# Kernel tuning notes

Measured on AMD Instinct MI355X. Metric: run time of the kernel, lower is better.

Reference implementation:

```python
import jax, jax.numpy as jnp
import numpy as np

EMBD = 512
HEADS = 8
HEAD = EMBD // HEADS


def setup_inputs() -> dict:
    key = jax.random.key(0)
    ks = jax.random.split(key, 9)
    B, M = 4, 2048
    s = 1.0 / np.sqrt(EMBD)
    inp = {
        "x": jax.random.normal(ks[0], (B, M, EMBD), dtype=jnp.float32),
        "wq": jax.random.uniform(ks[1], (EMBD, EMBD), jnp.float32, -s, s),
        "bq": jnp.zeros((EMBD,), jnp.float32),
        "wk": jax.random.uniform(ks[2], (EMBD, EMBD), jnp.float32, -s, s),
        "bk": jnp.zeros((EMBD,), jnp.float32),
        "wv": jax.random.uniform(ks[3], (EMBD, EMBD), jnp.float32, -s, s),
        "bv": jnp.zeros((EMBD,), jnp.float32),
        "wo": jax.random.uniform(ks[4], (EMBD, EMBD), jnp.float32, -s, s),
        "bo": jnp.zeros((EMBD,), jnp.float32),
        "gamma": jnp.ones((EMBD,), jnp.float32),
        "beta": jnp.zeros((EMBD,), jnp.float32),
    }
    return inp


def layer_norm(x, gamma, beta, eps=1e-5):
    mu = jnp.mean(x, axis=-1, keepdims=True)
    var = jnp.mean(jnp.square(x - mu), axis=-1, keepdims=True)
    return (x - mu) * jax.lax.rsqrt(var + eps) * gamma + beta


def reference(x, wq, bq, wk, bk, wv, bv, wo, bo, gamma, beta):
    B, M, _ = x.shape
    norm = layer_norm(x, gamma, beta)
    # projections; reshape to [B, H, M, Dh]
    def proj(w, b):
        return (norm @ w.T + b).reshape(B, M, HEADS, HEAD).transpose(0, 2, 1, 3)
    q = proj(wq, bq)
    k = proj(wk, bk)
    v = proj(wv, bv)
    scores = jnp.einsum("bhmd,bhnd->bhmn", q, k) / np.sqrt(HEAD)
    # exclude self-attention on the diagonal
    diag = jnp.eye(M, dtype=bool)
    scores = jnp.where(diag, -jnp.inf, scores)
    attn = jax.nn.softmax(scores, axis=-1)
    ctx = jnp.einsum("bhmn,bhnd->bhmd", attn, v)
    ctx = ctx.transpose(0, 2, 1, 3).reshape(B, M, EMBD)
    out = ctx @ wo.T + bo
    return (out + x, attn)
```

## Files before the change

kernel.cpp:

```cpp
#include <hip/hip_runtime.h>

#define B_   4
#define H_   8
#define M_   2048
#define D_   512
#define DH_  64

typedef short  bf16x8 __attribute__((ext_vector_type(8)));
typedef short  bf16x4 __attribute__((ext_vector_type(4)));
typedef float  f32x4  __attribute__((ext_vector_type(4)));
typedef unsigned short u16x4 __attribute__((ext_vector_type(4)));
typedef unsigned int   u32x2 __attribute__((ext_vector_type(2)));

#define EXPC 0.18033688011112042f

static __device__ __forceinline__ unsigned short f2bf(float f) {
  unsigned u = __float_as_uint(f);
  u += 0x7fffu + ((u >> 16) & 1u);
  return (unsigned short)(u >> 16);
}

static __device__ __forceinline__ unsigned cvtpk(float lo, float hi) {
  unsigned r;
  asm("v_cvt_pk_bf16_f32 %0, %1, %2" : "=v"(r) : "v"(lo), "v"(hi));
  return r;
}

static __device__ __forceinline__ f32x4 mfma16(bf16x4 a, bf16x4 b, f32x4 c) {
  asm("v_mfma_f32_16x16x16_bf16 %0, %1, %2, %0" : "+v"(c) : "v"(a), "v"(b));
  return c;
}

static __device__ __forceinline__ int swz128(int row, int byteoff) {
  return row * 128 + (byteoff ^ ((row & 7) << 4));
}

static __device__ __forceinline__ void glds16(const void* g, void* l) {
  __builtin_amdgcn_global_load_lds(
      (const __attribute__((address_space(1))) unsigned*)g,
      (__attribute__((address_space(3))) unsigned*)l, 16, 0, 0);
}

static __device__ __forceinline__ void stage_tile(
    const char* g0, size_t rstride, char* lds, int t) {
  const int r0 = t >> 3, c0 = t & 7;
  const char* src = g0 + (size_t)r0 * rstride + ((c0 ^ (r0 & 7)) << 4);
  char* dst = lds + ((t & 192) << 4);
  #pragma unroll
  for (int c = 0; c < 4; ++c)
    glds16(src + (size_t)c * 32 * rstride, dst + c * 4096);
}

static __device__ __forceinline__ void stage64(
    const char* g0, size_t rstride, char* lds, int t) {
  #pragma unroll
  for (int c = 0; c < 2; ++c) {
    int s = c * 256 + t;
    int row = s >> 3, ch = s & 7;
    const char* src = g0 + (size_t)row * rstride + ((ch ^ (row & 7)) << 4);
    glds16(src, lds + c * 4096 + ((t & 192) << 4));
  }
}

__global__ __launch_bounds__(256) void ln_kernel(
    const float* __restrict__ x, const float* __restrict__ gamma,
    const float* __restrict__ beta, unsigned short* __restrict__ xn)
{
  const int t = threadIdx.x;
  const int half = t >> 7;
  const int i = t & 127;
  const int row = blockIdx.x * 2 + half;

  f32x4 v = *(const f32x4*)(x + (size_t)row * D_ + i * 4);
  float s  = v[0] + v[1] + v[2] + v[3];
  float ss = v[0]*v[0] + v[1]*v[1] + v[2]*v[2] + v[3]*v[3];
  #pragma unroll
  for (int m = 1; m < 64; m <<= 1) {
    s  += __shfl_xor(s, m);
    ss += __shfl_xor(ss, m);
  }
  __shared__ float red[2][2][2];
  const int w = (i >> 6) & 1;
  if ((i & 63) == 0) { red[half][w][0] = s; red[half][w][1] = ss; }
  __syncthreads();
  s  = red[half][0][0] + red[half][1][0];
  ss = red[half][0][1] + red[half][1][1];
  float mu  = s * (1.0f / D_);
  float var = ss * (1.0f / D_) - mu * mu;
  float rstd = rsqrtf(var + 1e-5f);

  f32x4 g4 = *(const f32x4*)(gamma + i * 4);
  f32x4 b4 = *(const f32x4*)(beta  + i * 4);
  u32x2 u;
  u[0] = cvtpk((v[0] - mu) * rstd * g4[0] + b4[0],
               (v[1] - mu) * rstd * g4[1] + b4[1]);
  u[1] = cvtpk((v[2] - mu) * rstd * g4[2] + b4[2],
               (v[3] - mu) * rstd * g4[3] + b4[3]);
  *(u32x2*)(xn + (size_t)row * D_ + i * 4) = u;
}

__global__ __launch_bounds__(256) void cast_w_kernel(
    const float* __restrict__ wq, const float* __restrict__ wk,
    const float* __restrict__ wv, const float* __restrict__ wo,
    unsigned short* __restrict__ wqkv, unsigned short* __restrict__ wob)
{
  int i = blockIdx.x * 256 + threadIdx.x;
  wqkv[i]          = f2bf(wq[i]);
  wqkv[i + 262144] = f2bf(wk[i]);
  wqkv[i + 524288] = f2bf(wv[i]);
  wob[i]           = f2bf(wo[i]);
}

__global__ __launch_bounds__(256) void qkv_gemm(
    const unsigned short* __restrict__ xn,
    const unsigned short* __restrict__ wqkv,
    const float* __restrict__ bq, const float* __restrict__ bk,
    const float* __restrict__ bv,
    unsigned short* __restrict__ q, unsigned short* __restrict__ Kp,
    unsigned short* __restrict__ Vp)
{
  __shared__ __align__(16) char As[128 * 128];
  __shared__ __align__(16) char Bs[128 * 128];
  const int m0 = blockIdx.x * 128;
  const int n0 = blockIdx.y * 128;
  const int t = threadIdx.x, wid = t >> 6, lane = t & 63;
  const int wr = (wid >> 1) * 64, wc = (wid & 1) * 64;
  const int cl = lane & 15, rg = lane >> 4;
  const f32x4 z4 = {0.f, 0.f, 0.f, 0.f};
  const bool isv = (n0 >= 1024);

  const char* agb = (const char*)xn   + (size_t)m0 * 1024;
  const char* bgb = (const char*)wqkv + (size_t)n0 * 1024;

  f32x4 acc[4][4];
  #pragma unroll
  for (int i = 0; i < 4; ++i)
    #pragma unroll
    for (int j = 0; j < 4; ++j) acc[i][j] = z4;

  for (int k0 = 0; k0 < 512; k0 += 64) {
    __syncthreads();
    stage_tile(agb + k0 * 2, 1024, As, t);
    stage_tile(bgb + k0 * 2, 1024, Bs, t);
    __syncthreads();
    #pragma unroll
    for (int ks = 0; ks < 2; ++ks) {
      int koff = ks * 64 + rg * 16;
      bf16x8 af[4], bfr[4];
      #pragma unroll
      for (int i = 0; i < 4; ++i)
        af[i] = *(const bf16x8*)(As + swz128(wr + i * 16 + cl, koff));
      #pragma unroll
      for (int j = 0; j < 4; ++j)
        bfr[j] = *(const bf16x8*)(Bs + swz128(wc + j * 16 + cl, koff));
      if (isv) {
        #pragma unroll
        for (int i = 0; i < 4; ++i)
          #pragma unroll
          for (int j = 0; j < 4; ++j)
            acc[i][j] = __builtin_amdgcn_mfma_f32_16x16x32_bf16(af[i], bfr[j], acc[i][j], 0, 0, 0);
      } else {
        #pragma unroll
        for (int j = 0; j < 4; ++j)
          #pragma unroll
          for (int i = 0; i < 4; ++i)
            acc[j][i] = __builtin_amdgcn_mfma_f32_16x16x32_bf16(bfr[j], af[i], acc[j][i], 0, 0, 0);
      }
    }
  }

  if (isv) {
    #pragma unroll
    for (int j = 0; j < 4; ++j) {
      int n = n0 + wc + j * 16 + cl;
      int nn = n & 511;
      int h = nn >> 6, dh = nn & 63;
      int jd = dh >> 4, cld = dh & 15;
      float bias = bv[nn];
      #pragma unroll
      for (int i = 0; i < 4; ++i) {
        int mrow = m0 + wr + i * 16 + rg * 4;
        int b = mrow >> 11, mm = mrow & 2047;
        int nt = mm >> 6, nl = mm & 63;
        int jp = nl >> 5, half = (nl >> 4) & 1, rgv = (nl >> 2) & 3;
        u32x2 u;
        u[0] = cvtpk(acc[i][j][0] + bias, acc[i][j][1] + bias);
        u[1] = cvtpk(acc[i][j][2] + bias, acc[i][j][3] + bias);
        size_t off = ((((size_t)(b * H_ + h) * 32 + nt) * 4 + jd) * 2 + jp) * 512
                   + (rgv * 16 + cld) * 8 + half * 4;
        *(u16x4*)(Vp + off) = __builtin_bit_cast(u16x4, u);
      }
    }
  } else {
    const int mat = n0 >> 9;
    #pragma unroll
    for (int j = 0; j < 4; ++j) {
      int nn0 = ((n0 + wc) & 511) + j * 16 + rg * 4;
      int h = nn0 >> 6, dh = nn0 & 63;
      f32x4 b4 = *(const f32x4*)((mat ? bk : bq) + nn0);
      #pragma unroll
      for (int i = 0; i < 4; ++i) {
        int mrow = m0 + wr + i * 16 + cl;
        int b = mrow >> 11, mm = mrow & 2047;
        u32x2 u;
        u[0] = cvtpk(acc[j][i][0] + b4[0], acc[j][i][1] + b4[1]);
        u[1] = cvtpk(acc[j][i][2] + b4[2], acc[j][i][3] + b4[3]);
        if (mat == 0) {
          *(u16x4*)(q + ((size_t)(b * H_ + h) * M_ + mm) * DH_ + dh) =
              __builtin_bit_cast(u16x4, u);
        } else {
          int ks = dh >> 5, rgk = (dh >> 3) & 3, e0 = dh & 7;
          size_t off = ((((size_t)(b * H_ + h) * 32 + (mm >> 6)) * 4 + ((mm >> 4) & 3)) * 2 + ks) * 512
                     + (rgk * 16 + (mm & 15)) * 8 + e0;
          *(u16x4*)(Kp + off) = __builtin_bit_cast(u16x4, u);
        }
      }
    }
  }
}

__global__ __launch_bounds__(256, 4) void attn_kernel(
    const unsigned short* __restrict__ q,
    const unsigned short* __restrict__ Kp,
    const unsigned short* __restrict__ Vp,
    float* __restrict__ attn,
    unsigned short* __restrict__ ctx)
{
  __shared__ __align__(16) char Ps[4][2048];

  const int flat = blockIdx.x;
  const int bh = (flat & 7) * 4 + ((flat >> 3) >> 5);
  const int mb = (flat >> 3) & 31;
  const int m0 = mb * 64;
  const int t = threadIdx.x, wid = t >> 6, lane = t & 63;
  const int wr = wid * 16, cl = lane & 15, rg = lane >> 4;
  const int m_g = m0 + wr + cl;
  const f32x4 z4 = {0.f, 0.f, 0.f, 0.f};

  const char* qb = (const char*)(q + (size_t)bh * M_ * DH_);
  const unsigned short* kpb = Kp + (size_t)bh * 131072;
  const unsigned short* vpb = Vp + (size_t)bh * 131072;
  float* ab = attn + (size_t)bh * M_ * M_;

  bf16x8 qf[2];
  #pragma unroll
  for (int ks = 0; ks < 2; ++ks)
    qf[ks] = *(const bf16x8*)(qb + (size_t)m_g * 128 + ks * 64 + rg * 16);

  float psum = 0.f;
  for (int nt = 0; nt < 32; ++nt) {
    const unsigned short* kch = kpb + (size_t)nt * 4096;
    f32x4 s[4];
    #pragma unroll
    for (int j = 0; j < 4; ++j) s[j] = z4;
    #pragma unroll
    for (int ks = 0; ks < 2; ++ks)
      #pragma unroll
      for (int j = 0; j < 4; ++j) {
        bf16x8 kf = *(const bf16x8*)(kch + (j * 2 + ks) * 512 + lane * 8);
        s[j] = __builtin_amdgcn_mfma_f32_16x16x32_bf16(kf, qf[ks], s[j], 0, 0, 0);
      }
    if (nt == mb) {
      #pragma unroll
      for (int j = 0; j < 4; ++j)
        #pragma unroll
        for (int r = 0; r < 4; ++r) {
          int n_g = nt * 64 + j * 16 + rg * 4 + r;
          float p = __builtin_amdgcn_exp2f(s[j][r] * EXPC);
          psum += (n_g == m_g) ? 0.f : p;
        }
    } else {
      #pragma unroll
      for (int j = 0; j < 4; ++j)
        #pragma unroll
        for (int r = 0; r < 4; ++r)
          psum += __builtin_amdgcn_exp2f(s[j][r] * EXPC);
    }
  }
  psum += __shfl_xor(psum, 16);
  psum += __shfl_xor(psum, 32);
  const float rv = 1.0f / psum;

  f32x4 oc[4];
  #pragma unroll
  for (int j = 0; j < 4; ++j) oc[j] = z4;

  const int srow = lane >> 4;
  const int sch  = lane & 15;

  asm volatile("s_nop 7" :::);

  for (int nt = 0; nt < 32; ++nt) {
    const unsigned short* kch = kpb + (size_t)nt * 4096;
    const unsigned short* vch = vpb + (size_t)nt * 4096;
    f32x4 s[4];
    #pragma unroll
    for (int j = 0; j < 4; ++j) s[j] = z4;
    #pragma unroll
    for (int ks = 0; ks < 2; ++ks)
      #pragma unroll
      for (int j = 0; j < 4; ++j) {
        bf16x8 kf = *(const bf16x8*)(kch + (j * 2 + ks) * 512 + lane * 8);
        s[j] = __builtin_amdgcn_mfma_f32_16x16x32_bf16(kf, qf[ks], s[j], 0, 0, 0);
      }
    const bool dtile = (nt == mb);
    bf16x4 pb[4];
    #pragma unroll
    for (int j = 0; j < 4; ++j) {
      f32x4 pv;
      #pragma unroll
      for (int r = 0; r < 4; ++r) {
        int n_g = nt * 64 + j * 16 + rg * 4 + r;
        float p = __builtin_amdgcn_exp2f(s[j][r] * EXPC) * rv;
        pv[r] = (dtile && n_g == m_g) ? 0.f : p;
      }
      u32x2 uu;
      uu[0] = cvtpk(pv[0], pv[1]);
      uu[1] = cvtpk(pv[2], pv[3]);
      pb[j] = __builtin_bit_cast(bf16x4, uu);
      *(u32x2*)(Ps[wid] + swz128(cl, j * 32 + rg * 8)) = uu;
    }
    {
      float* abase = ab + ((size_t)(m0 + wr + srow)) * M_ + nt * 64 + sch * 4;
      #pragma unroll
      for (int it = 0; it < 4; ++it) {
        u16x4 pu = *(const u16x4*)(Ps[wid] + swz128(it * 4 + srow, sch * 8));
        f32x4 pv;
        #pragma unroll
        for (int r = 0; r < 4; ++r) pv[r] = __uint_as_float((unsigned)pu[r] << 16);
        __builtin_nontemporal_store(pv, (f32x4*)(abase + (size_t)it * 4 * M_));
      }
    }
    #pragma unroll
    for (int jp = 0; jp < 2; ++jp)
      #pragma unroll
      for (int jd = 0; jd < 4; ++jd) {
        bf16x8 w = *(const bf16x8*)(vch + (jd * 2 + jp) * 512 + lane * 8);
        bf16x4 vlo = __builtin_shufflevector(w, w, 0, 1, 2, 3);
        bf16x4 vhi = __builtin_shufflevector(w, w, 4, 5, 6, 7);
        oc[jd] = mfma16(vlo, pb[jp * 2],     oc[jd]);
        oc[jd] = mfma16(vhi, pb[jp * 2 + 1], oc[jd]);
      }
  }

  asm volatile("s_nop 7\n\ts_nop 7" :::);

  int b = bh >> 3, h = bh & 7;
  unsigned short* crow = ctx + ((size_t)b * M_ + m_g) * D_ + h * DH_ + rg * 4;
  #pragma unroll
  for (int jd = 0; jd < 4; ++jd) {
    u32x2 u;
    u[0] = cvtpk(oc[jd][0], oc[jd][1]);
    u[1] = cvtpk(oc[jd][2], oc[jd][3]);
    *(u32x2*)(crow + jd * 16) = u;
  }
}

__global__ __launch_bounds__(256) void out_gemm(
    const unsigned short* __restrict__ ctxb,
    const unsigned short* __restrict__ wob,
    const float* __restrict__ bo,
    const float* __restrict__ x,
    float* __restrict__ out)
{
  __shared__ __align__(16) char As[128 * 128];
  __shared__ __align__(16) char Bs[64 * 128];
  const int m0 = blockIdx.x * 128;
  const int n0 = blockIdx.y * 64;
  const int t = threadIdx.x, wid = t >> 6, lane = t & 63;
  const int wr = (wid >> 1) * 64, wc = (wid & 1) * 32;
  const int cl = lane & 15, rg = lane >> 4;
  const f32x4 z4 = {0.f, 0.f, 0.f, 0.f};

  const char* agb = (const char*)ctxb + (size_t)m0 * 1024;
  const char* bgb = (const char*)wob  + (size_t)n0 * 1024;

  f32x4 acc[2][4];
  #pragma unroll
  for (int j = 0; j < 2; ++j)
    #pragma unroll
    for (int i = 0; i < 4; ++i) acc[j][i] = z4;

  for (int k0 = 0; k0 < 512; k0 += 64) {
    __syncthreads();
    stage_tile(agb + k0 * 2, 1024, As, t);
    stage64(bgb + k0 * 2, 1024, Bs, t);
    __syncthreads();
    #pragma unroll
    for (int ks = 0; ks < 2; ++ks) {
      int koff = ks * 64 + rg * 16;
      bf16x8 af[4], bfr[2];
      #pragma unroll
      for (int i = 0; i < 4; ++i)
        af[i] = *(const bf16x8*)(As + swz128(wr + i * 16 + cl, koff));
      #pragma unroll
      for (int j = 0; j < 2; ++j)
        bfr[j] = *(const bf16x8*)(Bs + swz128(wc + j * 16 + cl, koff));
      #pragma unroll
      for (int j = 0; j < 2; ++j)
        #pragma unroll
        for (int i = 0; i < 4; ++i)
          acc[j][i] = __builtin_amdgcn_mfma_f32_16x16x32_bf16(bfr[j], af[i], acc[j][i], 0, 0, 0);
    }
  }

  #pragma unroll
  for (int j = 0; j < 2; ++j) {
    int nb = n0 + wc + j * 16 + rg * 4;
    f32x4 bo4 = *(const f32x4*)(bo + nb);
    #pragma unroll
    for (int i = 0; i < 4; ++i) {
      int m = m0 + wr + i * 16 + cl;
      f32x4 x4 = *(const f32x4*)(x + (size_t)m * 512 + nb);
      f32x4 o;
      #pragma unroll
      for (int r = 0; r < 4; ++r) o[r] = acc[j][i][r] + bo4[r] + x4[r];
      *(f32x4*)(out + (size_t)m * 512 + nb) = o;
    }
  }
}

extern "C" void kernel_launch(void* const* d_in, const int* in_sizes, int n_in,
                              void* d_out, int out_size, void* d_ws, size_t ws_size,
                              hipStream_t stream) {
  const float* x     = (const float*)d_in[0];
  const float* wq    = (const float*)d_in[1];
  const float* bq    = (const float*)d_in[2];
  const float* wk    = (const float*)d_in[3];
  const float* bk    = (const float*)d_in[4];
  const float* wv    = (const float*)d_in[5];
  const float* bv    = (const float*)d_in[6];
  const float* wo    = (const float*)d_in[7];
  const float* bo    = (const float*)d_in[8];
  const float* gamma = (const float*)d_in[9];
  const float* beta  = (const float*)d_in[10];

  char* ws = (char*)d_ws;
  unsigned short* xn   = (unsigned short*)(ws);
  unsigned short* wqkv = (unsigned short*)(ws + 8388608);
  unsigned short* wob  = (unsigned short*)(ws + 9961472);
  unsigned short* qb   = (unsigned short*)(ws + 10485760);
  unsigned short* Kp   = (unsigned short*)(ws + 18874368);
  unsigned short* Vp   = (unsigned short*)(ws + 27262976);
  unsigned short* ctx  = (unsigned short*)(ws + 35651584);

  float* out  = (float*)d_out;
  float* attn = (float*)d_out + 4194304;

  ln_kernel<<<4096, 256, 0, stream>>>(x, gamma, beta, xn);
  cast_w_kernel<<<1024, 256, 0, stream>>>(wq, wk, wv, wo, wqkv, wob);
  qkv_gemm<<<dim3(64, 12), 256, 0, stream>>>(xn, wqkv, bq, bk, bv, qb, Kp, Vp);
  attn_kernel<<<1024, 256, 0, stream>>>(qb, Kp, Vp, attn, ctx);
  out_gemm<<<dim3(64, 8), 256, 0, stream>>>(ctx, wob, bo, x, out);
}
```

Before: 198.3 us.

## Split softmax denominator pass into separate high-occupancy kernel

Moves the first pass of the attention kernel, which computes the exp-sum per row, into its own kernel with a higher occupancy launch bound. The result is stored as a reciprocal buffer in the workspace. The main kernel then reads it and performs only the write-out and PV pass. The aim is to let the compute-only pass run at higher occupancy without the register and LDS footprint of the second pass. The cost is an extra launch, a second read of Q, and a small global round trip.

```diff
diff --git a/kernel.cpp b/kernel.cpp
--- a/kernel.cpp
+++ b/kernel.cpp
@@ -219,15 +219,11 @@
   }
 }
 
-__global__ __launch_bounds__(256, 4) void attn_kernel(
+__global__ __launch_bounds__(256, 8) void psum_kernel(
     const unsigned short* __restrict__ q,
     const unsigned short* __restrict__ Kp,
-    const unsigned short* __restrict__ Vp,
-    float* __restrict__ attn,
-    unsigned short* __restrict__ ctx)
-{
-  __shared__ __align__(16) char Ps[4][2048];
-
+    float* __restrict__ rinv)
+{
   const int flat = blockIdx.x;
   const int bh = (flat & 7) * 4 + ((flat >> 3) >> 5);
   const int mb = (flat >> 3) & 31;
@@ -239,8 +235,6 @@
 
   const char* qb = (const char*)(q + (size_t)bh * M_ * DH_);
   const unsigned short* kpb = Kp + (size_t)bh * 131072;
-  const unsigned short* vpb = Vp + (size_t)bh * 131072;
-  float* ab = attn + (size_t)bh * M_ * M_;
 
   bf16x8 qf[2];
   #pragma unroll
@@ -279,7 +273,38 @@
   }
   psum += __shfl_xor(psum, 16);
   psum += __shfl_xor(psum, 32);
-  const float rv = 1.0f / psum;
+  if (lane < 16) rinv[bh * M_ + m_g] = 1.0f / psum;
+}
+
+__global__ __launch_bounds__(256, 4) void attn2_kernel(
+    const unsigned short* __restrict__ q,
+    const unsigned short* __restrict__ Kp,
+    const unsigned short* __restrict__ Vp,
+    const float* __restrict__ rinv,
+    float* __restrict__ attn,
+    unsigned short* __restrict__ ctx)
+{
+  __shared__ __align__(16) char Ps[4][2048];
+
+  const int flat = blockIdx.x;
+  const int bh = (flat & 7) * 4 + ((flat >> 3) >> 5);
+  const int mb = (flat >> 3) & 31;
+  const int m0 = mb * 64;
+  const int t = threadIdx.x, wid = t >> 6, lane = t & 63;
+  const int wr = wid * 16, cl = lane & 15, rg = lane >> 4;
+  const int m_g = m0 + wr + cl;
+  const f32x4 z4 = {0.f, 0.f, 0.f, 0.f};
+
+  const char* qb = (const char*)(q + (size_t)bh * M_ * DH_);
+  const unsigned short* kpb = Kp + (size_t)bh * 131072;
+  const unsigned short* vpb = Vp + (size_t)bh * 131072;
+  float* ab = attn + (size_t)bh * M_ * M_;
+
+  const float rv = rinv[bh * M_ + m_g];
+  bf16x8 qf[2];
+  #pragma unroll
+  for (int ks = 0; ks < 2; ++ks)
+    qf[ks] = *(const bf16x8*)(qb + (size_t)m_g * 128 + ks * 64 + rg * 16);
 
   f32x4 oc[4];
   #pragma unroll
@@ -443,6 +468,7 @@
   unsigned short* Kp   = (unsigned short*)(ws + 18874368);
   unsigned short* Vp   = (unsigned short*)(ws + 27262976);
   unsigned short* ctx  = (unsigned short*)(ws + 35651584);
+  float*          rinv = (float*)(ws + 44040192);
 
   float* out  = (float*)d_out;
   float* attn = (float*)d_out + 4194304;
@@ -450,6 +476,7 @@
   ln_kernel<<<4096, 256, 0, stream>>>(x, gamma, beta, xn);
   cast_w_kernel<<<1024, 256, 0, stream>>>(wq, wk, wv, wo, wqkv, wob);
   qkv_gemm<<<dim3(64, 12), 256, 0, stream>>>(xn, wqkv, bq, bk, bv, qb, Kp, Vp);
-  attn_kernel<<<1024, 256, 0, stream>>>(qb, Kp, Vp, attn, ctx);
+  psum_kernel<<<1024, 256, 0, stream>>>(qb, Kp, rinv);
+  attn2_kernel<<<1024, 256, 0, stream>>>(qb, Kp, Vp, rinv, attn, ctx);
   out_gemm<<<dim3(64, 8), 256, 0, stream>>>(ctx, wob, bo, x, out);
 }
```

After: 220.0 us. 1.11x slower.

## Split attention key range across two blocks and merge partial contexts in out GEMM

Applied to the files above, without the earlier changes.

Each attention block now handles half of the key tiles in the second (write/PV) pass, doubling the grid to 2048 blocks, and writes a partial context into one of two buffers. The xn workspace region is reused as the first buffer. The out-projection GEMM sums the two partial contexts in bf16 while staging its A tile, and the attention launch bound is raised to 8 blocks per CU. This aims for more parallelism and occupancy in the attention kernel. In exchange, the first pass that computes the full row sums is repeated by both halves, each output is rounded twice through bf16, and the A staging becomes plain loads plus adds.

```diff
diff --git a/kernel.cpp b/kernel.cpp
--- a/kernel.cpp
+++ b/kernel.cpp
@@ -11,6 +11,7 @@
 typedef float  f32x4  __attribute__((ext_vector_type(4)));
 typedef unsigned short u16x4 __attribute__((ext_vector_type(4)));
 typedef unsigned int   u32x2 __attribute__((ext_vector_type(2)));
+typedef unsigned int   u32x4 __attribute__((ext_vector_type(4)));
 
 #define EXPC 0.18033688011112042f
 
@@ -24,6 +25,14 @@
   unsigned r;
   asm("v_cvt_pk_bf16_f32 %0, %1, %2" : "=v"(r) : "v"(lo), "v"(hi));
   return r;
+}
+
+static __device__ __forceinline__ unsigned addbf2(unsigned a, unsigned b) {
+  float alo = __uint_as_float(a << 16);
+  float ahi = __uint_as_float(a & 0xffff0000u);
+  float blo = __uint_as_float(b << 16);
+  float bhi = __uint_as_float(b & 0xffff0000u);
+  return cvtpk(alo + blo, ahi + bhi);
 }
 
 static __device__ __forceinline__ f32x4 mfma16(bf16x4 a, bf16x4 b, f32x4 c) {
@@ -219,18 +228,22 @@
   }
 }
 
-__global__ __launch_bounds__(256, 4) void attn_kernel(
+__global__ __launch_bounds__(256, 8) void attn_kernel(
     const unsigned short* __restrict__ q,
     const unsigned short* __restrict__ Kp,
     const unsigned short* __restrict__ Vp,
     float* __restrict__ attn,
-    unsigned short* __restrict__ ctx)
+    unsigned short* __restrict__ ctxA,
+    unsigned short* __restrict__ ctxB)
 {
   __shared__ __align__(16) char Ps[4][2048];
 
   const int flat = blockIdx.x;
-  const int bh = (flat & 7) * 4 + ((flat >> 3) >> 5);
-  const int mb = (flat >> 3) & 31;
+  const int g = flat >> 3;
+  const int bh = (flat & 7) * 4 + (g >> 6);
+  const int rem = g & 63;
+  const int mb = rem >> 1;
+  const int half = rem & 1;
   const int m0 = mb * 64;
   const int t = threadIdx.x, wid = t >> 6, lane = t & 63;
   const int wr = wid * 16, cl = lane & 15, rg = lane >> 4;
@@ -287,10 +300,11 @@
 
   const int srow = lane >> 4;
   const int sch  = lane & 15;
+  const int nt0 = half * 16;
 
   asm volatile("s_nop 7" :::);
 
-  for (int nt = 0; nt < 32; ++nt) {
+  for (int nt = nt0; nt < nt0 + 16; ++nt) {
     const unsigned short* kch = kpb + (size_t)nt * 4096;
     const unsigned short* vch = vpb + (size_t)nt * 4096;
     f32x4 s[4];
@@ -346,7 +360,8 @@
   asm volatile("s_nop 7\n\ts_nop 7" :::);
 
   int b = bh >> 3, h = bh & 7;
-  unsigned short* crow = ctx + ((size_t)b * M_ + m_g) * D_ + h * DH_ + rg * 4;
+  unsigned short* ctxh = half ? ctxB : ctxA;
+  unsigned short* crow = ctxh + ((size_t)b * M_ + m_g) * D_ + h * DH_ + rg * 4;
   #pragma unroll
   for (int jd = 0; jd < 4; ++jd) {
     u32x2 u;
@@ -357,7 +372,8 @@
 }
 
 __global__ __launch_bounds__(256) void out_gemm(
-    const unsigned short* __restrict__ ctxb,
+    const unsigned short* __restrict__ ctxA,
+    const unsigned short* __restrict__ ctxB,
     const unsigned short* __restrict__ wob,
     const float* __restrict__ bo,
     const float* __restrict__ x,
@@ -372,19 +388,31 @@
   const int cl = lane & 15, rg = lane >> 4;
   const f32x4 z4 = {0.f, 0.f, 0.f, 0.f};
 
-  const char* agb = (const char*)ctxb + (size_t)m0 * 1024;
-  const char* bgb = (const char*)wob  + (size_t)n0 * 1024;
+  const char* aA = (const char*)ctxA + (size_t)m0 * 1024;
+  const char* aB = (const char*)ctxB + (size_t)m0 * 1024;
+  const char* bgb = (const char*)wob + (size_t)n0 * 1024;
 
   f32x4 acc[2][4];
   #pragma unroll
   for (int j = 0; j < 2; ++j)
     #pragma unroll
     for (int i = 0; i < 4; ++i) acc[j][i] = z4;
+
+  const int r0 = t >> 3, c0 = t & 7;
+  const size_t goff = (size_t)r0 * 1024 + ((c0 ^ (r0 & 7)) << 4);
 
   for (int k0 = 0; k0 < 512; k0 += 64) {
     __syncthreads();
-    stage_tile(agb + k0 * 2, 1024, As, t);
     stage64(bgb + k0 * 2, 1024, Bs, t);
+    #pragma unroll
+    for (int c = 0; c < 4; ++c) {
+      u32x4 a = *(const u32x4*)(aA + goff + (size_t)c * 32 * 1024 + k0 * 2);
+      u32x4 b = *(const u32x4*)(aB + goff + (size_t)c * 32 * 1024 + k0 * 2);
+      u32x4 o;
+      #pragma unroll
+      for (int e = 0; e < 4; ++e) o[e] = addbf2(a[e], b[e]);
+      *(u32x4*)(As + c * 4096 + t * 16) = o;
+    }
     __syncthreads();
     #pragma unroll
     for (int ks = 0; ks < 2; ++ks) {
@@ -437,12 +465,13 @@
 
   char* ws = (char*)d_ws;
   unsigned short* xn   = (unsigned short*)(ws);
+  unsigned short* ctxA = (unsigned short*)(ws);
   unsigned short* wqkv = (unsigned short*)(ws + 8388608);
   unsigned short* wob  = (unsigned short*)(ws + 9961472);
   unsigned short* qb   = (unsigned short*)(ws + 10485760);
   unsigned short* Kp   = (unsigned short*)(ws + 18874368);
   unsigned short* Vp   = (unsigned short*)(ws + 27262976);
-  unsigned short* ctx  = (unsigned short*)(ws + 35651584);
+  unsigned short* ctxB = (unsigned short*)(ws + 35651584);
 
   float* out  = (float*)d_out;
   float* attn = (float*)d_out + 4194304;
@@ -450,6 +479,6 @@
   ln_kernel<<<4096, 256, 0, stream>>>(x, gamma, beta, xn);
   cast_w_kernel<<<1024, 256, 0, stream>>>(wq, wk, wv, wo, wqkv, wob);
   qkv_gemm<<<dim3(64, 12), 256, 0, stream>>>(xn, wqkv, bq, bk, bv, qb, Kp, Vp);
-  attn_kernel<<<1024, 256, 0, stream>>>(qb, Kp, Vp, attn, ctx);
-  out_gemm<<<dim3(64, 8), 256, 0, stream>>>(ctx, wob, bo, x, out);
-}
+  attn_kernel<<<2048, 256, 0, stream>>>(qb, Kp, Vp, attn, ctxA, ctxB);
+  out_gemm<<<dim3(64, 8), 256, 0, stream>>>(ctxA, ctxB, wob, bo, x, out);
+}
```

After: 224.1 us. 1.13x slower.
